# Kernel optimization log

Hardware: AMD Instinct MI355X
Metric: run time of the kernel (lower is better)

The kernel has to match this reference:

```python
import jax, jax.numpy as jnp
import numpy as np

B, N, D, M, C = 4, 256, 128, 128, 128


def _lin_init(key, din, dout):
    # torch nn.Linear default: U(-1/sqrt(din), 1/sqrt(din)) for weight and bias
    bound = 1.0 / np.sqrt(din)
    kw, kb = jax.random.split(key)
    W = jax.random.uniform(kw, (din, dout), jnp.float32, -bound, bound)
    b = jax.random.uniform(kb, (dout,), jnp.float32, -bound, bound)
    return W, b


def setup_inputs() -> dict:
    key = jax.random.key(0)
    k_h, k_adj, k1, k2, k3, k4 = jax.random.split(key, 6)
    h = jax.random.normal(k_h, (B, N, D), jnp.float32)
    adj = jax.random.uniform(k_adj, (B, N, N), jnp.float32)
    # msg MLP: Linear(2D -> M), SiLU, Linear(M -> M). Split first weight into
    # the h_i block (W1a) and h_j block (W1b) of the concatenated input.
    W1, b1 = _lin_init(k1, 2 * D, M)
    W1a, W1b = W1[:D], W1[D:]
    W2, b2 = _lin_init(k2, M, M)
    # to_c MLP: Linear(M -> M), SiLU, Linear(M -> C)
    Wc1, bc1 = _lin_init(k3, M, M)
    Wc2, bc2 = _lin_init(k4, M, C)
    return {"h": h, "adj": adj, "W1a": W1a, "W1b": W1b, "b1": b1,
            "W2": W2, "b2": b2, "Wc1": Wc1, "bc1": bc1, "Wc2": Wc2, "bc2": bc2}


def reference(h, adj, W1a, W1b, b1, W2, b2, Wc1, bc1, Wc2, bc2):
    n = h.shape[1]
    # First msg Linear on cat([h_i, h_j]) == h_i @ W1a + h_j @ W1b + b1.
    # Precompute per-node projections once instead of the (B,N,N,2D) pair tensor.
    pi = jnp.einsum('bnd,dm->bnm', h, W1a)           # (B,N,M) for destination i
    pj = jnp.einsum('bnd,dm->bnm', h, W1b)           # (B,N,M) for source j
    pre = pi[:, :, None, :] + pj[:, None, :, :] + b1  # (B,N,N,M)
    m = jnp.einsum('bijm,mk->bijk', jax.nn.silu(pre), W2) + b2  # (B,N,N,M)
    # zero self-messages (diagonal ignored), then weight by adjacency
    mask = (1.0 - jnp.eye(n, dtype=h.dtype))[None, :, :, None]
    m = m * mask * adj[..., None]
    # mean aggregation over source nodes j with clamped degree
    denom = jnp.clip(jnp.sum(adj, axis=-1, keepdims=True), 1.0)  # (B,N,1)
    m_agg = jnp.sum(m, axis=2) / denom                           # (B,N,M)
    c = jnp.einsum('bnm,mc->bnc', jax.nn.silu(jnp.einsum('bnm,mk->bnk', m_agg, Wc1) + bc1), Wc2) + bc2
    return c
```

## Files before the change

### kernel.cpp

```cpp
#include <hip/hip_runtime.h>
#include <math.h>

#define BB 4
#define NN 256
#define DD 128
#define MM 128
#define CC 128
#define ROWS (BB * NN)
#define RPB 4
#define NBLK (ROWS / RPB)
#define TPB 512

#define L2E 1.44269504088896340736f

#define WS_PIB   0
#define WS_PJLO  131072
#define WS_PJHI  196608
#define WS_W2T   262144
#define WS_WC1T  278528
#define WS_WC2T  294912

static __device__ __forceinline__ float fast_exp2(float x) {
#if __has_builtin(__builtin_amdgcn_exp2f)
    return __builtin_amdgcn_exp2f(x);
#else
    return __exp2f(x);
#endif
}

static __device__ __forceinline__ float fast_rcp(float x) {
#if __has_builtin(__builtin_amdgcn_rcpf)
    return __builtin_amdgcn_rcpf(x);
#else
    return 1.0f / x;
#endif
}

static __device__ __forceinline__ float silu_f(float x) {
    float e = fast_exp2(-L2E * x);
    return x * fast_rcp(1.0f + e);
}

#if __has_builtin(__builtin_amdgcn_global_load_lds)
#define HAS_GLDS 1
#define GLDS(gp, lp)                                                        \
    __builtin_amdgcn_global_load_lds(                                       \
        (const __attribute__((address_space(1))) void*)(gp),                \
        (__attribute__((address_space(3))) void*)(lp), 16, 0, 0)
#else
#define HAS_GLDS 0
#endif

template <int ITERS>
static __device__ __forceinline__ void stage_lin(float* lds, const float* g,
                                                 int t) {
#if HAS_GLDS
    const int wv = t >> 6, lane = t & 63;
    #pragma unroll
    for (int i = 0; i < ITERS; ++i) {
        const int c = i * 8 + wv;
        GLDS(g + (size_t)c * 256 + lane * 4, lds + c * 256);
    }
#else
    #pragma unroll
    for (int i = 0; i < ITERS; ++i)
        ((float4*)lds)[i * TPB + t] = ((const float4*)g)[i * TPB + t];
#endif
}

__global__ __launch_bounds__(TPB) void k_proj(const float* __restrict__ h,
                                              const float* __restrict__ W1a,
                                              const float* __restrict__ W1b,
                                              const float* __restrict__ b1,
                                              const float* __restrict__ W2,
                                              const float* __restrict__ Wc1,
                                              const float* __restrict__ Wc2,
                                              float* __restrict__ ws) {
    __shared__ __align__(16) float sW[128 * 256];
    __shared__ float sH[RPB * DD];

    const int t = threadIdx.x;
    const int m = t & 127;
    const int q = t >> 7;
    const int row0 = blockIdx.x * RPB;

    sH[t] = h[(size_t)row0 * DD + t];

#if HAS_GLDS
    {
        const int wv = t >> 6, lane = t & 63;
        #pragma unroll
        for (int i = 0; i < 16; ++i) {
            const int r = i * 8 + wv;
            const float* g = (lane < 32)
                                 ? (W1a + (size_t)r * 128 + lane * 4)
                                 : (W1b + (size_t)r * 128 + (lane - 32) * 4);
            GLDS(g, &sW[r * 256]);
        }
    }
#else
    #pragma unroll
    for (int i = 0; i < 16; ++i) {
        const int f = i * TPB + t;
        const int r = f >> 6;
        const int c4 = f & 63;
        const float4 v = (c4 < 32)
                             ? ((const float4*)(W1a + (size_t)r * 128))[c4]
                             : ((const float4*)(W1b + (size_t)r * 128))[c4 - 32];
        ((float4*)sW)[f] = v;
    }
#endif

    const float bias = b1[m];
    __syncthreads();

    float accA = 0.0f, accB = 0.0f;
    const float* sHq = &sH[q * DD];
    #pragma unroll 8
    for (int d = 0; d < 128; d += 2) {
        const float2 hv = *(const float2*)&sHq[d];
        accA = fmaf(hv.x, sW[d * 256 + m], accA);
        accB = fmaf(hv.x, sW[d * 256 + 128 + m], accB);
        accA = fmaf(hv.y, sW[(d + 1) * 256 + m], accA);
        accB = fmaf(hv.y, sW[(d + 1) * 256 + 128 + m], accB);
    }

    ws[WS_PIB + (size_t)row0 * MM + t] = accA + bias;

    {
        const int b    = row0 >> 8;
        const int jloc = (row0 & 255) + q;
        const int half = jloc >> 7;
        const int jj   = jloc & 127;
        const int c16  = jj >> 2;
        const int off  = (half ? WS_PJHI : WS_PJLO) + b * 16384 + m * 128 +
                         (((c16 ^ (m & 7)) << 2) | (jj & 3));
        ws[off] = accB;
    }

    if (blockIdx.x < 12) {
        const int blk = blockIdx.x;
        const float* Wsrc = (blk < 4) ? W2 : (blk < 8) ? Wc1 : Wc2;
        float* Wdst = ws + ((blk < 4) ? WS_W2T : (blk < 8) ? WS_WC1T : WS_WC2T);
        const int d0 = (blk & 3) * 32;
        const int k = m;
        #pragma unroll
        for (int i = 0; i < 8; ++i) {
            const int d = d0 + (q << 3) + i;
            const float v = Wsrc[(size_t)d * 128 + k];
            Wdst[k * 128 + ((((d >> 2) ^ (k & 7)) << 2) | (d & 3))] = v;
        }
    }
}

__global__ __launch_bounds__(TPB) void k_msgout(const float* __restrict__ adj,
                                                const float* __restrict__ b2,
                                                const float* __restrict__ bc1,
                                                const float* __restrict__ bc2,
                                                const float* __restrict__ ws,
                                                float* __restrict__ out) {
    __shared__ __align__(16) float sLo[16384];
    __shared__ __align__(16) float sHi[16384];
    __shared__ __align__(16) float sS[RPB * MM];
    __shared__ __align__(16) float sB[RPB * MM];
    __shared__ float sWr0[8], sWr1[8];

    const int t = threadIdx.x;
    const int blk = blockIdx.x;
    const int b = blk >> 6;
    const int i0 = (blk & 63) * RPB;
    const int row0 = b * NN + i0;

    const int m = t & 127;
    const int q = t >> 7;
    const int w = t >> 6;
    const int swz = m & 7;

    stage_lin<8>(sLo, ws + WS_PJLO + b * 16384, t);
    stage_lin<8>(sHi, ws + WS_PJHI + b * 16384, t);

    const float pim  = ws[WS_PIB + (size_t)row0 * MM + t];
    const float b2k  = b2[m];
    const float bc1k = bc1[m];
    const float bc2k = bc2[m];

    const float* arow = adj + (size_t)row0 * NN;
    const float a0v = arow[t];
    const float a1v = arow[t + TPB];
    float v0 = a0v, v1 = a1v;
    #pragma unroll
    for (int off = 32; off > 0; off >>= 1) {
        v0 += __shfl_xor(v0, off, 64);
        v1 += __shfl_xor(v1, off, 64);
    }
    if ((t & 63) == 0) { sWr0[w] = v0; sWr1[w] = v1; }

    const int srow = __builtin_amdgcn_readfirstlane(row0 + q);
    const float* __restrict__ adjr = adj + (size_t)srow * NN;

    __syncthreads();

    float A;
    {
        const int base = (q & 1) * 4;
        A = (q < 2) ? (sWr0[base] + sWr0[base + 1] + sWr0[base + 2] + sWr0[base + 3])
                    : (sWr1[base] + sWr1[base + 1] + sWr1[base + 2] + sWr1[base + 3]);
    }
    const float aii = adjr[srow & 255];
    const float inv = 1.0f / fmaxf(A, 1.0f);
    const float bet = (A - aii) * inv;
    const float npim = -L2E * pim;

    float acc;
    {
        const int iloc = i0 + q;
        const int jj = iloc & 127;
        const float* base = (iloc < 128) ? sLo : sHi;
        const float pjd = base[m * 128 + ((((jj >> 2) ^ swz) << 2) | (jj & 3))];
        acc = -aii * silu_f(pim + pjd);
    }

    const float* rowLo = sLo + m * 128;
    #pragma unroll 8
    for (int j4 = 0; j4 < 32; ++j4) {
        const float4 pv = *(const float4*)(rowLo + ((j4 ^ swz) << 2));
        const float4 av = *(const float4*)(adjr + (j4 << 2));
        const float x0 = pim + pv.x, x1 = pim + pv.y;
        const float x2 = pim + pv.z, x3 = pim + pv.w;
        const float e0 = fast_exp2(fmaf(-L2E, pv.x, npim));
        const float e1 = fast_exp2(fmaf(-L2E, pv.y, npim));
        const float e2 = fast_exp2(fmaf(-L2E, pv.z, npim));
        const float e3 = fast_exp2(fmaf(-L2E, pv.w, npim));
        const float d0 = 1.0f + e0, d1 = 1.0f + e1;
        const float d2 = 1.0f + e2, d3 = 1.0f + e3;
        const float r01 = fast_rcp(d0 * d1), r23 = fast_rcp(d2 * d3);
        acc = fmaf(av.x * x0, r01 * d1, acc);
        acc = fmaf(av.y * x1, r01 * d0, acc);
        acc = fmaf(av.z * x2, r23 * d3, acc);
        acc = fmaf(av.w * x3, r23 * d2, acc);
    }

    __syncthreads();
    stage_lin<8>(sLo, ws + WS_W2T, t);

    const float* rowHi = sHi + m * 128;
    #pragma unroll 8
    for (int j4 = 0; j4 < 32; ++j4) {
        const float4 pv = *(const float4*)(rowHi + ((j4 ^ swz) << 2));
        const float4 av = *(const float4*)(adjr + 128 + (j4 << 2));
        const float x0 = pim + pv.x, x1 = pim + pv.y;
        const float x2 = pim + pv.z, x3 = pim + pv.w;
        const float e0 = fast_exp2(fmaf(-L2E, pv.x, npim));
        const float e1 = fast_exp2(fmaf(-L2E, pv.y, npim));
        const float e2 = fast_exp2(fmaf(-L2E, pv.z, npim));
        const float e3 = fast_exp2(fmaf(-L2E, pv.w, npim));
        const float d0 = 1.0f + e0, d1 = 1.0f + e1;
        const float d2 = 1.0f + e2, d3 = 1.0f + e3;
        const float r01 = fast_rcp(d0 * d1), r23 = fast_rcp(d2 * d3);
        acc = fmaf(av.x * x0, r01 * d1, acc);
        acc = fmaf(av.y * x1, r01 * d0, acc);
        acc = fmaf(av.z * x2, r23 * d3, acc);
        acc = fmaf(av.w * x3, r23 * d2, acc);
    }
    sS[(q << 7) + m] = acc * inv;

    __syncthreads();
    stage_lin<8>(sHi, ws + WS_WC1T, t);

    float acc2 = bet * b2k;
    {
        const float* rw = sLo + m * 128;
        #pragma unroll 8
        for (int d4 = 0; d4 < 32; ++d4) {
            const float4 wv4 = *(const float4*)(rw + ((d4 ^ swz) << 2));
            const float4 sv4 = *(const float4*)(&sS[(q << 7) + (d4 << 2)]);
            acc2 = fmaf(sv4.x, wv4.x, acc2);
            acc2 = fmaf(sv4.y, wv4.y, acc2);
            acc2 = fmaf(sv4.z, wv4.z, acc2);
            acc2 = fmaf(sv4.w, wv4.w, acc2);
        }
    }
    sB[(q << 7) + m] = acc2;

    __syncthreads();
    stage_lin<8>(sLo, ws + WS_WC2T, t);

    acc2 = bc1k;
    {
        const float* rw = sHi + m * 128;
        #pragma unroll 8
        for (int d4 = 0; d4 < 32; ++d4) {
            const float4 wv4 = *(const float4*)(rw + ((d4 ^ swz) << 2));
            const float4 sv4 = *(const float4*)(&sB[(q << 7) + (d4 << 2)]);
            acc2 = fmaf(sv4.x, wv4.x, acc2);
            acc2 = fmaf(sv4.y, wv4.y, acc2);
            acc2 = fmaf(sv4.z, wv4.z, acc2);
            acc2 = fmaf(sv4.w, wv4.w, acc2);
        }
    }
    sS[(q << 7) + m] = silu_f(acc2);

    __syncthreads();

    acc2 = bc2k;
    {
        const float* rw = sLo + m * 128;
        #pragma unroll 8
        for (int d4 = 0; d4 < 32; ++d4) {
            const float4 wv4 = *(const float4*)(rw + ((d4 ^ swz) << 2));
            const float4 sv4 = *(const float4*)(&sS[(q << 7) + (d4 << 2)]);
            acc2 = fmaf(sv4.x, wv4.x, acc2);
            acc2 = fmaf(sv4.y, wv4.y, acc2);
            acc2 = fmaf(sv4.z, wv4.z, acc2);
            acc2 = fmaf(sv4.w, wv4.w, acc2);
        }
    }
    out[(size_t)row0 * CC + t] = acc2;
}

extern "C" void kernel_launch(void* const* d_in, const int* in_sizes, int n_in,
                              void* d_out, int out_size, void* d_ws, size_t ws_size,
                              hipStream_t stream) {
    const float* h   = (const float*)d_in[0];
    const float* adj = (const float*)d_in[1];
    const float* W1a = (const float*)d_in[2];
    const float* W1b = (const float*)d_in[3];
    const float* b1  = (const float*)d_in[4];
    const float* W2  = (const float*)d_in[5];
    const float* b2  = (const float*)d_in[6];
    const float* Wc1 = (const float*)d_in[7];
    const float* bc1 = (const float*)d_in[8];
    const float* Wc2 = (const float*)d_in[9];
    const float* bc2 = (const float*)d_in[10];
    float* out = (float*)d_out;
    float* ws  = (float*)d_ws;

    k_proj<<<NBLK, TPB, 0, stream>>>(h, W1a, W1b, b1, W2, Wc1, Wc2, ws);
    k_msgout<<<NBLK, TPB, 0, stream>>>(adj, b2, bc1, bc2, ws, out);
}
```

Before: 97.65 us.

## Split reduction dimension across threads in projection and output MLP matvecs

The projection kernel no longer stages the full W1a/W1b weights (128 KB) into shared memory. Instead each thread reads weights directly from global memory for a 64-wide slice of the input dimension, computes all four rows, and partial sums are combined through a small shared buffer. The three small matvecs at the end of the message kernel likewise split the 128-long reduction across the four thread groups, reusing each weight read for four rows and reducing through shared memory. This cuts shared-memory footprint and weight re-reads, at the cost of extra barriers and reduction steps.

```diff
diff --git a/kernel.cpp b/kernel.cpp
--- a/kernel.cpp
+++ b/kernel.cpp
@@ -76,77 +76,79 @@
                                               const float* __restrict__ Wc1,
                                               const float* __restrict__ Wc2,
                                               float* __restrict__ ws) {
-    __shared__ __align__(16) float sW[128 * 256];
-    __shared__ float sH[RPB * DD];
+    __shared__ __align__(16) float sH[RPB * DD];
+    __shared__ __align__(16) float sRed[256 * 20];
 
     const int t = threadIdx.x;
-    const int m = t & 127;
-    const int q = t >> 7;
+    const int m   = t & 127;
+    const int X   = (t >> 7) & 1;
+    const int dup = t >> 8;
     const int row0 = blockIdx.x * RPB;
 
     sH[t] = h[(size_t)row0 * DD + t];
-
-#if HAS_GLDS
-    {
-        const int wv = t >> 6, lane = t & 63;
-        #pragma unroll
-        for (int i = 0; i < 16; ++i) {
-            const int r = i * 8 + wv;
-            const float* g = (lane < 32)
-                                 ? (W1a + (size_t)r * 128 + lane * 4)
-                                 : (W1b + (size_t)r * 128 + (lane - 32) * 4);
-            GLDS(g, &sW[r * 256]);
-        }
-    }
-#else
-    #pragma unroll
-    for (int i = 0; i < 16; ++i) {
-        const int f = i * TPB + t;
-        const int r = f >> 6;
-        const int c4 = f & 63;
-        const float4 v = (c4 < 32)
-                             ? ((const float4*)(W1a + (size_t)r * 128))[c4]
-                             : ((const float4*)(W1b + (size_t)r * 128))[c4 - 32];
-        ((float4*)sW)[f] = v;
-    }
-#endif
-
+    const float* __restrict__ Wp = X ? W1b : W1a;
     const float bias = b1[m];
     __syncthreads();
 
-    float accA = 0.0f, accB = 0.0f;
-    const float* sHq = &sH[q * DD];
-    #pragma unroll 8
-    for (int d = 0; d < 128; d += 2) {
-        const float2 hv = *(const float2*)&sHq[d];
-        accA = fmaf(hv.x, sW[d * 256 + m], accA);
-        accB = fmaf(hv.x, sW[d * 256 + 128 + m], accB);
-        accA = fmaf(hv.y, sW[(d + 1) * 256 + m], accA);
-        accB = fmaf(hv.y, sW[(d + 1) * 256 + 128 + m], accB);
-    }
-
-    ws[WS_PIB + (size_t)row0 * MM + t] = accA + bias;
-
-    {
-        const int b    = row0 >> 8;
-        const int jloc = (row0 & 255) + q;
-        const int half = jloc >> 7;
-        const int jj   = jloc & 127;
-        const int c16  = jj >> 2;
-        const int off  = (half ? WS_PJHI : WS_PJLO) + b * 16384 + m * 128 +
-                         (((c16 ^ (m & 7)) << 2) | (jj & 3));
-        ws[off] = accB;
+    const int d0 = dup * 64;
+    float a0 = 0.f, a1 = 0.f, a2 = 0.f, a3 = 0.f;
+    #pragma unroll 4
+    for (int c = 0; c < 16; ++c) {
+        const int d = d0 + c * 4;
+        const float w0 = Wp[(size_t)(d + 0) * MM + m];
+        const float w1 = Wp[(size_t)(d + 1) * MM + m];
+        const float w2 = Wp[(size_t)(d + 2) * MM + m];
+        const float w3 = Wp[(size_t)(d + 3) * MM + m];
+        const float4 h0 = *(const float4*)&sH[0 * DD + d];
+        const float4 h1 = *(const float4*)&sH[1 * DD + d];
+        const float4 h2 = *(const float4*)&sH[2 * DD + d];
+        const float4 h3 = *(const float4*)&sH[3 * DD + d];
+        a0 = fmaf(h0.x, w0, a0); a0 = fmaf(h0.y, w1, a0);
+        a0 = fmaf(h0.z, w2, a0); a0 = fmaf(h0.w, w3, a0);
+        a1 = fmaf(h1.x, w0, a1); a1 = fmaf(h1.y, w1, a1);
+        a1 = fmaf(h1.z, w2, a1); a1 = fmaf(h1.w, w3, a1);
+        a2 = fmaf(h2.x, w0, a2); a2 = fmaf(h2.y, w1, a2);
+        a2 = fmaf(h2.z, w2, a2); a2 = fmaf(h2.w, w3, a2);
+        a3 = fmaf(h3.x, w0, a3); a3 = fmaf(h3.y, w1, a3);
+        a3 = fmaf(h3.z, w2, a3); a3 = fmaf(h3.w, w3, a3);
+    }
+    {
+        float4 pv; pv.x = a0; pv.y = a1; pv.z = a2; pv.w = a3;
+        *(float4*)&sRed[((X << 7) | m) * 20 + dup * 8] = pv;
+    }
+    __syncthreads();
+
+    {
+        const int base = ((X << 7) | m) * 20;
+        #pragma unroll
+        for (int k = 0; k < 2; ++k) {
+            const int q = 2 * dup + k;
+            const float v = sRed[base + q] + sRed[base + 8 + q];
+            if (X == 0) {
+                ws[WS_PIB + (size_t)(row0 + q) * MM + m] = v + bias;
+            } else {
+                const int b    = row0 >> 8;
+                const int jloc = (row0 & 255) + q;
+                const int half = jloc >> 7;
+                const int jj   = jloc & 127;
+                const int c16  = jj >> 2;
+                const int off  = (half ? WS_PJHI : WS_PJLO) + b * 16384 +
+                                 m * 128 + (((c16 ^ (m & 7)) << 2) | (jj & 3));
+                ws[off] = v;
+            }
+        }
     }
 
     if (blockIdx.x < 12) {
         const int blk = blockIdx.x;
+        const int qq = t >> 7;
         const float* Wsrc = (blk < 4) ? W2 : (blk < 8) ? Wc1 : Wc2;
         float* Wdst = ws + ((blk < 4) ? WS_W2T : (blk < 8) ? WS_WC1T : WS_WC2T);
-        const int d0 = (blk & 3) * 32;
+        const int d0t = (blk & 3) * 32;
         const int k = m;
         #pragma unroll
         for (int i = 0; i < 8; ++i) {
-            const int d = d0 + (q << 3) + i;
+            const int d = d0t + (qq << 3) + i;
             const float v = Wsrc[(size_t)d * 128 + k];
             Wdst[k * 128 + ((((d >> 2) ^ (k & 7)) << 2) | (d & 3))] = v;
         }
@@ -163,6 +165,7 @@
     __shared__ __align__(16) float sHi[16384];
     __shared__ __align__(16) float sS[RPB * MM];
     __shared__ __align__(16) float sB[RPB * MM];
+    __shared__ __align__(16) float sP[128 * 20];
     __shared__ float sWr0[8], sWr1[8];
 
     const int t = threadIdx.x;
@@ -267,55 +270,105 @@
     __syncthreads();
     stage_lin<8>(sHi, ws + WS_WC1T, t);
 
-    float acc2 = bet * b2k;
+
     {
         const float* rw = sLo + m * 128;
-        #pragma unroll 8
-        for (int d4 = 0; d4 < 32; ++d4) {
+        float p0 = 0.f, p1 = 0.f, p2 = 0.f, p3 = 0.f;
+        #pragma unroll
+        for (int i = 0; i < 8; ++i) {
+            const int d4 = (q << 3) + i;
             const float4 wv4 = *(const float4*)(rw + ((d4 ^ swz) << 2));
-            const float4 sv4 = *(const float4*)(&sS[(q << 7) + (d4 << 2)]);
-            acc2 = fmaf(sv4.x, wv4.x, acc2);
-            acc2 = fmaf(sv4.y, wv4.y, acc2);
-            acc2 = fmaf(sv4.z, wv4.z, acc2);
-            acc2 = fmaf(sv4.w, wv4.w, acc2);
-        }
-    }
-    sB[(q << 7) + m] = acc2;
-
+            const float4 s0 = *(const float4*)(&sS[(0 << 7) + (d4 << 2)]);
+            const float4 s1 = *(const float4*)(&sS[(1 << 7) + (d4 << 2)]);
+            const float4 s2 = *(const float4*)(&sS[(2 << 7) + (d4 << 2)]);
+            const float4 s3 = *(const float4*)(&sS[(3 << 7) + (d4 << 2)]);
+            p0 = fmaf(s0.x, wv4.x, p0); p0 = fmaf(s0.y, wv4.y, p0);
+            p0 = fmaf(s0.z, wv4.z, p0); p0 = fmaf(s0.w, wv4.w, p0);
+            p1 = fmaf(s1.x, wv4.x, p1); p1 = fmaf(s1.y, wv4.y, p1);
+            p1 = fmaf(s1.z, wv4.z, p1); p1 = fmaf(s1.w, wv4.w, p1);
+            p2 = fmaf(s2.x, wv4.x, p2); p2 = fmaf(s2.y, wv4.y, p2);
+            p2 = fmaf(s2.z, wv4.z, p2); p2 = fmaf(s2.w, wv4.w, p2);
+            p3 = fmaf(s3.x, wv4.x, p3); p3 = fmaf(s3.y, wv4.y, p3);
+            p3 = fmaf(s3.z, wv4.z, p3); p3 = fmaf(s3.w, wv4.w, p3);
+        }
+        float4 pv; pv.x = p0; pv.y = p1; pv.z = p2; pv.w = p3;
+        *(float4*)&sP[m * 20 + (q << 2)] = pv;
+    }
+    __syncthreads();
+
+    {
+        const int base = m * 20 + q;
+        const float mg = sP[base] + sP[base + 4] + sP[base + 8] + sP[base + 12]
+                         + bet * b2k;
+        sB[(q << 7) + m] = mg;
+    }
     __syncthreads();
     stage_lin<8>(sLo, ws + WS_WC2T, t);
 
-    acc2 = bc1k;
     {
         const float* rw = sHi + m * 128;
-        #pragma unroll 8
-        for (int d4 = 0; d4 < 32; ++d4) {
+        float p0 = 0.f, p1 = 0.f, p2 = 0.f, p3 = 0.f;
+        #pragma unroll
+        for (int i = 0; i < 8; ++i) {
+            const int d4 = (q << 3) + i;
             const float4 wv4 = *(const float4*)(rw + ((d4 ^ swz) << 2));
-            const float4 sv4 = *(const float4*)(&sB[(q << 7) + (d4 << 2)]);
-            acc2 = fmaf(sv4.x, wv4.x, acc2);
-            acc2 = fmaf(sv4.y, wv4.y, acc2);
-            acc2 = fmaf(sv4.z, wv4.z, acc2);
-            acc2 = fmaf(sv4.w, wv4.w, acc2);
-        }
-    }
-    sS[(q << 7) + m] = silu_f(acc2);
-
-    __syncthreads();
-
-    acc2 = bc2k;
+            const float4 s0 = *(const float4*)(&sB[(0 << 7) + (d4 << 2)]);
+            const float4 s1 = *(const float4*)(&sB[(1 << 7) + (d4 << 2)]);
+            const float4 s2 = *(const float4*)(&sB[(2 << 7) + (d4 << 2)]);
+            const float4 s3 = *(const float4*)(&sB[(3 << 7) + (d4 << 2)]);
+            p0 = fmaf(s0.x, wv4.x, p0); p0 = fmaf(s0.y, wv4.y, p0);
+            p0 = fmaf(s0.z, wv4.z, p0); p0 = fmaf(s0.w, wv4.w, p0);
+            p1 = fmaf(s1.x, wv4.x, p1); p1 = fmaf(s1.y, wv4.y, p1);
+            p1 = fmaf(s1.z, wv4.z, p1); p1 = fmaf(s1.w, wv4.w, p1);
+            p2 = fmaf(s2.x, wv4.x, p2); p2 = fmaf(s2.y, wv4.y, p2);
+            p2 = fmaf(s2.z, wv4.z, p2); p2 = fmaf(s2.w, wv4.w, p2);
+            p3 = fmaf(s3.x, wv4.x, p3); p3 = fmaf(s3.y, wv4.y, p3);
+            p3 = fmaf(s3.z, wv4.z, p3); p3 = fmaf(s3.w, wv4.w, p3);
+        }
+        float4 pv; pv.x = p0; pv.y = p1; pv.z = p2; pv.w = p3;
+        *(float4*)&sP[m * 20 + (q << 2)] = pv;
+    }
+    __syncthreads();
+
+    {
+        const int base = m * 20 + q;
+        const float tv = sP[base] + sP[base + 4] + sP[base + 8] + sP[base + 12]
+                         + bc1k;
+        sS[(q << 7) + m] = silu_f(tv);
+    }
+    __syncthreads();
+
     {
         const float* rw = sLo + m * 128;
-        #pragma unroll 8
-        for (int d4 = 0; d4 < 32; ++d4) {
+        float p0 = 0.f, p1 = 0.f, p2 = 0.f, p3 = 0.f;
+        #pragma unroll
+        for (int i = 0; i < 8; ++i) {
+            const int d4 = (q << 3) + i;
             const float4 wv4 = *(const float4*)(rw + ((d4 ^ swz) << 2));
-            const float4 sv4 = *(const float4*)(&sS[(q << 7) + (d4 << 2)]);
-            acc2 = fmaf(sv4.x, wv4.x, acc2);
-            acc2 = fmaf(sv4.y, wv4.y, acc2);
-            acc2 = fmaf(sv4.z, wv4.z, acc2);
-            acc2 = fmaf(sv4.w, wv4.w, acc2);
-        }
-    }
-    out[(size_t)row0 * CC + t] = acc2;
+            const float4 s0 = *(const float4*)(&sS[(0 << 7) + (d4 << 2)]);
+            const float4 s1 = *(const float4*)(&sS[(1 << 7) + (d4 << 2)]);
+            const float4 s2 = *(const float4*)(&sS[(2 << 7) + (d4 << 2)]);
+            const float4 s3 = *(const float4*)(&sS[(3 << 7) + (d4 << 2)]);
+            p0 = fmaf(s0.x, wv4.x, p0); p0 = fmaf(s0.y, wv4.y, p0);
+            p0 = fmaf(s0.z, wv4.z, p0); p0 = fmaf(s0.w, wv4.w, p0);
+            p1 = fmaf(s1.x, wv4.x, p1); p1 = fmaf(s1.y, wv4.y, p1);
+            p1 = fmaf(s1.z, wv4.z, p1); p1 = fmaf(s1.w, wv4.w, p1);
+            p2 = fmaf(s2.x, wv4.x, p2); p2 = fmaf(s2.y, wv4.y, p2);
+            p2 = fmaf(s2.z, wv4.z, p2); p2 = fmaf(s2.w, wv4.w, p2);
+            p3 = fmaf(s3.x, wv4.x, p3); p3 = fmaf(s3.y, wv4.y, p3);
+            p3 = fmaf(s3.z, wv4.z, p3); p3 = fmaf(s3.w, wv4.w, p3);
+        }
+        float4 pv; pv.x = p0; pv.y = p1; pv.z = p2; pv.w = p3;
+        *(float4*)&sP[m * 20 + (q << 2)] = pv;
+    }
+    __syncthreads();
+
+    {
+        const int base = m * 20 + q;
+        const float ov = sP[base] + sP[base + 4] + sP[base + 8] + sP[base + 12]
+                         + bc2k;
+        out[(size_t)row0 * CC + t] = ov;
+    }
 }
 
 extern "C" void kernel_launch(void* const* d_in, const int* in_sizes, int n_in,
```

New measurement: 96.50 us. Within noise of the previous version (-1.2%).
